# Performance work log

Hardware: AMD Instinct MI355X
Metric: run time of the kernel (lower is better)

Reference implementation:

```python
import jax, jax.numpy as jnp
import numpy as np

K = 3          # neighbors for interpolation (torch_geometric default)
BIG = 1e10     # masks cross-batch pairs out of the kNN search
EPS = 1e-16    # clamp on squared distance before inverting (PyG knn_interpolate)


def setup_inputs() -> dict:
    key = jax.random.key(0)
    ks = jax.random.split(key, 8)
    N, M, C_IN, C_SKIP, H = 4096, 16384, 256, 128, 256
    x = jax.random.normal(ks[0], (N, C_IN), dtype=jnp.float32)
    pos = jax.random.normal(ks[1], (N, 3), dtype=jnp.float32)
    batch = jnp.zeros((N,), dtype=jnp.int64)
    x_skip = jax.random.normal(ks[2], (M, C_SKIP), dtype=jnp.float32)
    pos_skip = jax.random.normal(ks[3], (M, 3), dtype=jnp.float32)
    batch_skip = jnp.zeros((M,), dtype=jnp.int64)
    # MLP params: Linear(384->256) + ReLU + Linear(256->256)
    W1 = jax.random.normal(ks[4], (C_IN + C_SKIP, H), dtype=jnp.float32) * (1.0 / np.sqrt(C_IN + C_SKIP))
    b1 = jnp.zeros((H,), dtype=jnp.float32)
    W2 = jax.random.normal(ks[5], (H, H), dtype=jnp.float32) * (1.0 / np.sqrt(H))
    b2 = jnp.zeros((H,), dtype=jnp.float32)
    return {"x": x, "pos": pos, "batch": batch, "x_skip": x_skip,
            "pos_skip": pos_skip, "batch_skip": batch_skip,
            "W1": W1, "b1": b1, "W2": W2, "b2": b2}


def knn_interpolate(x, pos, pos_skip, batch, batch_skip, k):
    # squared pairwise distances [M, N] via ||q||^2 + ||p||^2 - 2 q.p (avoids [M,N,3])
    qq = jnp.sum(pos_skip * pos_skip, axis=1, keepdims=True)      # [M,1]
    pp = jnp.sum(pos * pos, axis=1)                               # [N]
    d2 = qq + pp[None, :] - 2.0 * (pos_skip @ pos.T)              # [M,N]
    d2 = d2 + jnp.where(batch_skip[:, None] != batch[None, :], BIG, 0.0)
    _, idx = jax.lax.top_k(-d2, k)                                # [M,k] nearest indices
    # recompute exact squared distances for the chosen neighbors
    nbr_pos = pos[idx]                                            # [M,k,3]
    d2k = jnp.sum((pos_skip[:, None, :] - nbr_pos) ** 2, axis=-1) # [M,k]
    w = 1.0 / jnp.clip(d2k, EPS)                                  # inverse-distance weights
    nbr_x = x[idx]                                                # [M,k,C]
    y = jnp.einsum('mk,mkc->mc', w, nbr_x) / jnp.sum(w, axis=1, keepdims=True)
    return y


def reference(x, pos, batch, x_skip, pos_skip, batch_skip, W1, b1, W2, b2):
    y = knn_interpolate(x, pos, pos_skip, batch, batch_skip, K)   # [M, C_in]
    h = jnp.concatenate([y, x_skip], axis=1)                      # [M, C_in+C_skip]
    h = jax.nn.relu(h @ W1 + b1)
    out = h @ W2 + b2
    return (out, pos_skip, batch_skip)
```

## Files before the change

kernel.cpp:

```cpp
#include <hip/hip_runtime.h>
#include <hip/hip_bf16.h>

#define N_PTS  4096
#define M_Q    16384
#define C_IN   256
#define C_SKIP 128
#define C_H    384
#define HDIM   256
#define QB     64

typedef __bf16 bf16x8 __attribute__((ext_vector_type(8)));
typedef float  f32x4  __attribute__((ext_vector_type(4)));

__device__ __forceinline__ void insert3(float d, int j,
                                        float& b0, float& b1, float& b2,
                                        int& i0, int& i1, int& i2) {
    if (d < b2) {
        if (d < b1) {
            b2 = b1; i2 = i1;
            if (d < b0) { b1 = b0; i1 = i0; b0 = d; i0 = j; }
            else        { b1 = d;  i1 = j; }
        } else { b2 = d; i2 = j; }
    }
}

__global__ __launch_bounds__(256) void prep_tail_kernel(
        const float* __restrict__ W1, const float* __restrict__ W2,
        const float* __restrict__ pos, const float* __restrict__ pos_skip,
        __hip_bfloat16* __restrict__ W1t, __hip_bfloat16* __restrict__ W2t,
        float4* __restrict__ pos4, float* __restrict__ out, int out_size) {
    const int i = blockIdx.x * 256 + threadIdx.x;
    if (i < C_H * HDIM) {
        const int k = i / HDIM, n = i % HDIM;
        W1t[n * C_H + k] = __float2bfloat16(W1[i]);
    } else if (i < C_H * HDIM + HDIM * HDIM) {
        const int j = i - C_H * HDIM;
        const int k = j / HDIM, n = j % HDIM;
        W2t[n * HDIM + k] = __float2bfloat16(W2[j]);
    } else if (i < C_H * HDIM + HDIM * HDIM + N_PTS) {
        const int j = i - (C_H * HDIM + HDIM * HDIM);
        const float px = pos[j*3+0], py = pos[j*3+1], pz = pos[j*3+2];
        pos4[j] = make_float4(px, py, pz, px*px + py*py + pz*pz);
    }
    if (i < M_Q * 3) out[(size_t)M_Q * HDIM + i] = pos_skip[i];
    const int zbase = M_Q * HDIM + M_Q * 3;
    if (zbase + i < out_size) out[zbase + i] = 0.0f;
}

__global__ __launch_bounds__(512) void mega_kernel(
        const float4* __restrict__ pos4, const float* __restrict__ pos_skip,
        const float* __restrict__ x, const float* __restrict__ x_skip,
        const __bf16* __restrict__ W1t, const __bf16* __restrict__ W2t,
        const float* __restrict__ b1, const float* __restrict__ b2,
        float* __restrict__ out) {
    __shared__ __align__(16) char smem[51712];
    __hip_bfloat16* h     = (__hip_bfloat16*)smem;
    __hip_bfloat16* hid   = (__hip_bfloat16*)smem;
    float*          candD = (float*)smem;
    int*            candI = (int*)  (smem + 6144);
    int*            idxL  = (int*)  (smem + 50176);
    float*          wnL   = (float*)(smem + 50944);

    const int t    = threadIdx.x;
    const int m0   = blockIdx.x * QB;
    const int wave = t >> 6, lane = t & 63;

    float4 skipv[4];
    #pragma unroll
    for (int p = 0; p < 4; ++p) {
        const int g = p * 512 + t;
        const int r = g >> 5, c = (g & 31) * 4;
        skipv[p] = *(const float4*)(x_skip + (size_t)(m0 + r) * C_SKIP + c);
    }

    const int q = m0 + lane;
    const float qx = pos_skip[q*3+0], qy = pos_skip[q*3+1], qz = pos_skip[q*3+2];
    const float m2x = -2.0f * qx, m2y = -2.0f * qy, m2z = -2.0f * qz;

    {
        const int j0 = __builtin_amdgcn_readfirstlane(wave * (N_PTS / 8));
        float bb0 = 3e38f, bb1 = 3e38f, bb2 = 3e38f;
        int   ii0 = 0, ii1 = 0, ii2 = 0;
        #pragma unroll 8
        for (int j = 0; j < N_PTS / 8; ++j) {
            const float4 p = pos4[j0 + j];
            const float d = fmaf(p.x, m2x, fmaf(p.y, m2y, fmaf(p.z, m2z, p.w)));
            const int  jj = j0 + j;
            const bool c0 = d < bb0, c1 = d < bb1, c2 = d < bb2;
            ii2 = c2 ? (c1 ? ii1 : jj) : ii2;
            ii1 = c1 ? (c0 ? ii0 : jj) : ii1;
            ii0 = c0 ? jj : ii0;
            bb2 = __builtin_amdgcn_fmed3f(d, bb1, bb2);
            bb1 = __builtin_amdgcn_fmed3f(d, bb0, bb1);
            bb0 = fminf(bb0, d);
        }
        const int ci = (wave * 64 + lane) * 3;
        candD[ci+0] = bb0; candD[ci+1] = bb1; candD[ci+2] = bb2;
        candI[ci+0] = ii0; candI[ci+1] = ii1; candI[ci+2] = ii2;
    }
    __syncthreads();

    if (t < 64) {
        float B0 = 3e38f, B1 = 3e38f, B2v = 3e38f;
        int   I0 = 0, I1 = 0, I2 = 0;
        #pragma unroll
        for (int ww = 0; ww < 8; ++ww) {
            const int ci = (ww * 64 + t) * 3;
            insert3(candD[ci+0], candI[ci+0], B0,B1,B2v, I0,I1,I2);
            insert3(candD[ci+1], candI[ci+1], B0,B1,B2v, I0,I1,I2);
            insert3(candD[ci+2], candI[ci+2], B0,B1,B2v, I0,I1,I2);
        }
        const float qq = qx*qx + qy*qy + qz*qz;
        const float w0 = 1.0f / fmaxf(B0  + qq, 1e-16f);
        const float w1 = 1.0f / fmaxf(B1  + qq, 1e-16f);
        const float w2 = 1.0f / fmaxf(B2v + qq, 1e-16f);
        const float inv = 1.0f / (w0 + w1 + w2);
        idxL[t*3+0] = I0; idxL[t*3+1] = I1; idxL[t*3+2] = I2;
        wnL[t*3+0] = w0*inv; wnL[t*3+1] = w1*inv; wnL[t*3+2] = w2*inv;
    }
    __syncthreads();

    const int ln = lane & 15, kq = lane >> 4;
    const int wm  = (wave >> 2) * 32;
    const int wnc = (wave & 3) * 64;

    bf16x8 bfA[4], bfB[4];
    #pragma unroll
    for (int nt = 0; nt < 4; ++nt) {
        bfA[nt] = *(const bf16x8*)(W1t + (size_t)(wnc + nt*16 + ln) * C_H +  0 + kq*8);
        bfB[nt] = *(const bf16x8*)(W1t + (size_t)(wnc + nt*16 + ln) * C_H + 32 + kq*8);
    }

    #pragma unroll
    for (int p = 0; p < 4; ++p) {
        const int g = p * 512 + t;
        const int r = g >> 5, c = (g & 31) * 4;
        union { __hip_bfloat162 v2[2]; uint2 u; } pk;
        pk.v2[0].x = __float2bfloat16(skipv[p].x); pk.v2[0].y = __float2bfloat16(skipv[p].y);
        pk.v2[1].x = __float2bfloat16(skipv[p].z); pk.v2[1].y = __float2bfloat16(skipv[p].w);
        *(uint2*)&h[(size_t)r * 392 + C_IN + c] = pk.u;
    }
    #pragma unroll 4
    for (int p = 0; p < 8; ++p) {
        const int g = p * 512 + t;
        const int r = g >> 6, c = (g & 63) * 4;
        const int   i0 = idxL[r*3+0], i1 = idxL[r*3+1], i2 = idxL[r*3+2];
        const float w0 = wnL[r*3+0],  w1 = wnL[r*3+1],  w2 = wnL[r*3+2];
        const float4 v0 = *(const float4*)(x + (size_t)i0 * C_IN + c);
        const float4 v1 = *(const float4*)(x + (size_t)i1 * C_IN + c);
        const float4 v2 = *(const float4*)(x + (size_t)i2 * C_IN + c);
        union { __hip_bfloat162 v2_[2]; uint2 u; } pk;
        pk.v2_[0].x = __float2bfloat16(w0*v0.x + w1*v1.x + w2*v2.x);
        pk.v2_[0].y = __float2bfloat16(w0*v0.y + w1*v1.y + w2*v2.y);
        pk.v2_[1].x = __float2bfloat16(w0*v0.z + w1*v1.z + w2*v2.z);
        pk.v2_[1].y = __float2bfloat16(w0*v0.w + w1*v1.w + w2*v2.w);
        *(uint2*)&h[(size_t)r * 392 + c] = pk.u;
    }
    __syncthreads();

    f32x4 acc[2][4] = {};

    #pragma unroll
    for (int s = 0; s < 12; ++s) {
        const int k0 = s * 32;
        bf16x8* bc = (s & 1) ? bfB : bfA;
        const bf16x8 a0 = *(const bf16x8*)&h[(size_t)(wm +      ln) * 392 + k0 + kq*8];
        const bf16x8 a1 = *(const bf16x8*)&h[(size_t)(wm + 16 + ln) * 392 + k0 + kq*8];
        #pragma unroll
        for (int nt = 0; nt < 4; ++nt)
            acc[0][nt] = __builtin_amdgcn_mfma_f32_16x16x32_bf16(a0, bc[nt], acc[0][nt], 0,0,0);
        #pragma unroll
        for (int nt = 0; nt < 4; ++nt)
            acc[1][nt] = __builtin_amdgcn_mfma_f32_16x16x32_bf16(a1, bc[nt], acc[1][nt], 0,0,0);
        if (s < 10) {
            #pragma unroll
            for (int nt = 0; nt < 4; ++nt)
                bc[nt] = *(const bf16x8*)(W1t + (size_t)(wnc + nt*16 + ln) * C_H + (k0 + 64) + kq*8);
        } else {
            #pragma unroll
            for (int nt = 0; nt < 4; ++nt)
                bc[nt] = *(const bf16x8*)(W2t + (size_t)(wnc + nt*16 + ln) * HDIM + (s - 10) * 32 + kq*8);
        }
    }
    __syncthreads();

    #pragma unroll
    for (int nt = 0; nt < 4; ++nt) {
        const int n = wnc + nt*16 + ln;
        const float bv = b1[n];
        #pragma unroll
        for (int mt = 0; mt < 2; ++mt) {
            const int rbase = wm + mt*16 + kq*4;
            #pragma unroll
            for (int r = 0; r < 4; ++r) {
                const float v = fmaxf(acc[mt][nt][r] + bv, 0.0f);
                hid[(size_t)(rbase + r) * 264 + n] = __float2bfloat16(v);
                acc[mt][nt][r] = 0.0f;
            }
        }
    }
    __syncthreads();

    #pragma unroll
    for (int s = 0; s < 8; ++s) {
        const int k0 = s * 32;
        bf16x8* bc = (s & 1) ? bfB : bfA;
        const bf16x8 a0 = *(const bf16x8*)&hid[(size_t)(wm +      ln) * 264 + k0 + kq*8];
        const bf16x8 a1 = *(const bf16x8*)&hid[(size_t)(wm + 16 + ln) * 264 + k0 + kq*8];
        #pragma unroll
        for (int nt = 0; nt < 4; ++nt)
            acc[0][nt] = __builtin_amdgcn_mfma_f32_16x16x32_bf16(a0, bc[nt], acc[0][nt], 0,0,0);
        #pragma unroll
        for (int nt = 0; nt < 4; ++nt)
            acc[1][nt] = __builtin_amdgcn_mfma_f32_16x16x32_bf16(a1, bc[nt], acc[1][nt], 0,0,0);
        if (s < 6) {
            #pragma unroll
            for (int nt = 0; nt < 4; ++nt)
                bc[nt] = *(const bf16x8*)(W2t + (size_t)(wnc + nt*16 + ln) * HDIM + (k0 + 64) + kq*8);
        }
    }

    #pragma unroll
    for (int nt = 0; nt < 4; ++nt) {
        const int n = wnc + nt*16 + ln;
        const float bv = b2[n];
        #pragma unroll
        for (int mt = 0; mt < 2; ++mt) {
            const int rbase = m0 + wm + mt*16 + kq*4;
            #pragma unroll
            for (int r = 0; r < 4; ++r)
                out[(size_t)(rbase + r) * HDIM + n] = acc[mt][nt][r] + bv;
        }
    }
}

extern "C" void kernel_launch(void* const* d_in, const int* in_sizes, int n_in,
                              void* d_out, int out_size, void* d_ws, size_t ws_size,
                              hipStream_t stream) {
    (void)in_sizes; (void)n_in; (void)ws_size;
    const float* x        = (const float*)d_in[0];
    const float* pos      = (const float*)d_in[1];
    const float* x_skip   = (const float*)d_in[3];
    const float* pos_skip = (const float*)d_in[4];
    const float* W1       = (const float*)d_in[6];
    const float* b1       = (const float*)d_in[7];
    const float* W2       = (const float*)d_in[8];
    const float* b2       = (const float*)d_in[9];
    float* out = (float*)d_out;

    char* ws = (char*)d_ws;
    __hip_bfloat16* W1t  = (__hip_bfloat16*)(ws);
    __hip_bfloat16* W2t  = (__hip_bfloat16*)(ws + 196608);
    float4*         pos4 = (float4*)(ws + 327680);

    prep_tail_kernel<<<(C_H*HDIM + HDIM*HDIM + N_PTS + 255)/256, 256, 0, stream>>>(
        W1, W2, pos, pos_skip, W1t, W2t, pos4, out, out_size);
    mega_kernel<<<M_Q/QB, 512, 0, stream>>>(
        pos4, pos_skip, x, x_skip, (const __bf16*)W1t, (const __bf16*)W2t, b1, b2, out);
}
```

Before: 151.4 us.

## Compute kNN distances with bf16-split MFMA and two-pass exact candidate refinement

Replaces the scalar FMA distance scan with MFMA matrix products. Coordinates are split into three bf16 parts to approximate fp32 precision, and the packed query and point operands are built in the prep kernel. A first pass finds an approximate third-nearest distance per query. A second pass collects every point within that threshold plus a margin into a shared-memory candidate list, and the final top-3 is recomputed with exact fp32 distances. This is meant to move the dominant distance work onto matrix cores, but it scans the points twice and relies on the margin and candidate cap of 24 to keep results correct.

```diff
diff --git a/kernel.cpp b/kernel.cpp
--- a/kernel.cpp
+++ b/kernel.cpp
@@ -8,39 +8,83 @@
 #define C_H    384
 #define HDIM   256
 #define QB     64
+#define CANDMAX 24
+#define EPSW   4e-3f
 
 typedef __bf16 bf16x8 __attribute__((ext_vector_type(8)));
 typedef float  f32x4  __attribute__((ext_vector_type(4)));
 
-__device__ __forceinline__ void insert3(float d, int j,
-                                        float& b0, float& b1, float& b2,
-                                        int& i0, int& i1, int& i2) {
-    if (d < b2) {
-        if (d < b1) {
-            b2 = b1; i2 = i1;
-            if (d < b0) { b1 = b0; i1 = i0; b0 = d; i0 = j; }
-            else        { b1 = d;  i1 = j; }
-        } else { b2 = d; i2 = j; }
-    }
+#define PW1  (C_H*HDIM)
+#define PW2  (PW1 + HDIM*HDIM)
+#define PPV  (PW2 + N_PTS)
+#define PAQ  (PPV + M_Q)
+
+__device__ __forceinline__ unsigned short bfbits(float v) {
+    __hip_bfloat16 b = __float2bfloat16(v);
+    return *(unsigned short*)&b;
+}
+__device__ __forceinline__ float bff(unsigned short u) {
+    __hip_bfloat16 b = *(__hip_bfloat16*)&u;
+    return __bfloat162float(b);
+}
+__device__ __forceinline__ void split3(float v, unsigned short& h,
+                                       unsigned short& m, unsigned short& l) {
+    h = bfbits(v);       float r  = v - bff(h);
+    m = bfbits(r);       float r2 = r - bff(m);
+    l = bfbits(r2);
 }
 
 __global__ __launch_bounds__(256) void prep_tail_kernel(
         const float* __restrict__ W1, const float* __restrict__ W2,
         const float* __restrict__ pos, const float* __restrict__ pos_skip,
         __hip_bfloat16* __restrict__ W1t, __hip_bfloat16* __restrict__ W2t,
-        float4* __restrict__ pos4, float* __restrict__ out, int out_size) {
+        __hip_bfloat16* __restrict__ Aq, __hip_bfloat16* __restrict__ Pv,
+        float* __restrict__ out, int out_size) {
     const int i = blockIdx.x * 256 + threadIdx.x;
-    if (i < C_H * HDIM) {
+    if (i < PW1) {
         const int k = i / HDIM, n = i % HDIM;
         W1t[n * C_H + k] = __float2bfloat16(W1[i]);
-    } else if (i < C_H * HDIM + HDIM * HDIM) {
-        const int j = i - C_H * HDIM;
+    } else if (i < PW2) {
+        const int j = i - PW1;
         const int k = j / HDIM, n = j % HDIM;
         W2t[n * HDIM + k] = __float2bfloat16(W2[j]);
-    } else if (i < C_H * HDIM + HDIM * HDIM + N_PTS) {
-        const int j = i - (C_H * HDIM + HDIM * HDIM);
+    } else if (i < PPV) {
+        const int j = i - PW2;
         const float px = pos[j*3+0], py = pos[j*3+1], pz = pos[j*3+2];
-        pos4[j] = make_float4(px, py, pz, px*px + py*py + pz*pz);
+        const float pw = px*px + py*py + pz*pz;
+        union { unsigned short u[32]; uint4 q[4]; } S;
+        #pragma unroll
+        for (int k = 0; k < 32; ++k) S.u[k] = 0;
+        const float pd[3] = {px, py, pz};
+        #pragma unroll
+        for (int d = 0; d < 3; ++d) {
+            unsigned short bh, bm, bl; split3(pd[d], bh, bm, bl);
+            S.u[6*d+0] = bh; S.u[6*d+1] = bm; S.u[6*d+2] = bh;
+            S.u[6*d+3] = bl; S.u[6*d+4] = bh; S.u[6*d+5] = bm;
+        }
+        unsigned short wh, wm, wl; split3(pw, wh, wm, wl);
+        S.u[18] = wh; S.u[19] = wm; S.u[20] = wl;
+        uint4* dst = (uint4*)(Pv + (size_t)j * 32);
+        dst[0] = S.q[0]; dst[1] = S.q[1]; dst[2] = S.q[2]; dst[3] = S.q[3];
+    } else if (i < PAQ) {
+        const int j = i - PPV;
+        const float ax = -2.0f * pos_skip[j*3+0];
+        const float ay = -2.0f * pos_skip[j*3+1];
+        const float az = -2.0f * pos_skip[j*3+2];
+        union { unsigned short u[32]; uint4 q[4]; } S;
+        #pragma unroll
+        for (int k = 0; k < 32; ++k) S.u[k] = 0;
+        const float ad[3] = {ax, ay, az};
+        #pragma unroll
+        for (int d = 0; d < 3; ++d) {
+            unsigned short ah, am, al; split3(ad[d], ah, am, al);
+            S.u[6*d+0] = ah; S.u[6*d+1] = ah; S.u[6*d+2] = am;
+            S.u[6*d+3] = ah; S.u[6*d+4] = al; S.u[6*d+5] = am;
+        }
+        const unsigned short one = bfbits(1.0f);
+        S.u[18] = one; S.u[19] = one; S.u[20] = one;
+        uint4* dst = (uint4*)(Aq + (size_t)j * 32);
+        dst[0] = S.q[0]; dst[1] = S.q[1]; dst[2] = S.q[2]; dst[3] = S.q[3];
     }
     if (i < M_Q * 3) out[(size_t)M_Q * HDIM + i] = pos_skip[i];
     const int zbase = M_Q * HDIM + M_Q * 3;
@@ -48,22 +92,28 @@
 }
 
 __global__ __launch_bounds__(512) void mega_kernel(
-        const float4* __restrict__ pos4, const float* __restrict__ pos_skip,
+        const __bf16* __restrict__ Aq, const __bf16* __restrict__ Pv,
+        const float* __restrict__ pos, const float* __restrict__ pos_skip,
         const float* __restrict__ x, const float* __restrict__ x_skip,
         const __bf16* __restrict__ W1t, const __bf16* __restrict__ W2t,
         const float* __restrict__ b1, const float* __restrict__ b2,
         float* __restrict__ out) {
-    __shared__ __align__(16) char smem[51712];
+    __shared__ __align__(16) char smem[51968];
     __hip_bfloat16* h     = (__hip_bfloat16*)smem;
     __hip_bfloat16* hid   = (__hip_bfloat16*)smem;
     float*          candD = (float*)smem;
     int*            candI = (int*)  (smem + 6144);
-    int*            idxL  = (int*)  (smem + 50176);
-    float*          wnL   = (float*)(smem + 50944);
+    int*            candC = (int*)  (smem + 12288);
+    float*          bb2G  = (float*)(smem + 50176);
+    int*            idxL  = (int*)  (smem + 50432);
+    float*          wnL   = (float*)(smem + 51200);
 
     const int t    = threadIdx.x;
     const int m0   = blockIdx.x * QB;
     const int wave = t >> 6, lane = t & 63;
+    const int ln = lane & 15, kq = lane >> 4;
+
+    if (t < 64) candC[t] = 0;
 
     float4 skipv[4];
     #pragma unroll
@@ -73,54 +123,150 @@
         skipv[p] = *(const float4*)(x_skip + (size_t)(m0 + r) * C_SKIP + c);
     }
 
-    const int q = m0 + lane;
-    const float qx = pos_skip[q*3+0], qy = pos_skip[q*3+1], qz = pos_skip[q*3+2];
-    const float m2x = -2.0f * qx, m2y = -2.0f * qy, m2z = -2.0f * qz;
-
-    {
-        const int j0 = __builtin_amdgcn_readfirstlane(wave * (N_PTS / 8));
-        float bb0 = 3e38f, bb1 = 3e38f, bb2 = 3e38f;
-        int   ii0 = 0, ii1 = 0, ii2 = 0;
-        #pragma unroll 8
-        for (int j = 0; j < N_PTS / 8; ++j) {
-            const float4 p = pos4[j0 + j];
-            const float d = fmaf(p.x, m2x, fmaf(p.y, m2y, fmaf(p.z, m2z, p.w)));
-            const int  jj = j0 + j;
-            const bool c0 = d < bb0, c1 = d < bb1, c2 = d < bb2;
-            ii2 = c2 ? (c1 ? ii1 : jj) : ii2;
-            ii1 = c1 ? (c0 ? ii0 : jj) : ii1;
-            ii0 = c0 ? jj : ii0;
-            bb2 = __builtin_amdgcn_fmed3f(d, bb1, bb2);
-            bb1 = __builtin_amdgcn_fmed3f(d, bb0, bb1);
-            bb0 = fminf(bb0, d);
-        }
-        const int ci = (wave * 64 + lane) * 3;
-        candD[ci+0] = bb0; candD[ci+1] = bb1; candD[ci+2] = bb2;
-        candI[ci+0] = ii0; candI[ci+1] = ii1; candI[ci+2] = ii2;
+    bf16x8 afq[4];
+    #pragma unroll
+    for (int qt = 0; qt < 4; ++qt)
+        afq[qt] = *(const bf16x8*)(Aq + (size_t)(m0 + qt*16 + ln) * 32 + kq*8);
+
+    const f32x4 zacc = {0.0f, 0.0f, 0.0f, 0.0f};
+    const int ptbase = wave * 32;
+
+    float b0_[4][4], b1_[4][4], b2_[4][4];
+    #pragma unroll
+    for (int qt = 0; qt < 4; ++qt)
+        #pragma unroll
+        for (int r = 0; r < 4; ++r) { b0_[qt][r]=3e38f; b1_[qt][r]=3e38f; b2_[qt][r]=3e38f; }
+
+    bf16x8 bcur = *(const bf16x8*)(Pv + (size_t)(ptbase*16 + ln) * 32 + kq*8);
+    for (int pt = 0; pt < 32; ++pt) {
+        bf16x8 bnext;
+        if (pt < 31)
+            bnext = *(const bf16x8*)(Pv + (size_t)((ptbase+pt+1)*16 + ln) * 32 + kq*8);
+        #pragma unroll
+        for (int qt = 0; qt < 4; ++qt) {
+            const f32x4 d = __builtin_amdgcn_mfma_f32_16x16x32_bf16(afq[qt], bcur, zacc, 0,0,0);
+            #pragma unroll
+            for (int r = 0; r < 4; ++r) {
+                b2_[qt][r] = __builtin_amdgcn_fmed3f(d[r], b1_[qt][r], b2_[qt][r]);
+                b1_[qt][r] = __builtin_amdgcn_fmed3f(d[r], b0_[qt][r], b1_[qt][r]);
+                b0_[qt][r] = fminf(b0_[qt][r], d[r]);
+            }
+        }
+        bcur = bnext;
+    }
+    #pragma unroll
+    for (int qt = 0; qt < 4; ++qt)
+        #pragma unroll
+        for (int r = 0; r < 4; ++r) {
+            float v0 = b0_[qt][r], v1 = b1_[qt][r], v2 = b2_[qt][r];
+            #pragma unroll
+            for (int m = 1; m <= 8; m <<= 1) {
+                const float o0 = __shfl_xor(v0, m), o1 = __shfl_xor(v1, m), o2 = __shfl_xor(v2, m);
+                const float mx  = fmaxf(v0, o0);
+                const float z0  = fminf(v0, o0);
+                const float mn1 = fminf(v1, o1);
+                const float mn2 = fminf(v2, o2);
+                v0 = z0;
+                v1 = fminf(mx, mn1);
+                v2 = __builtin_amdgcn_fmed3f(mx, mn1, mn2);
+            }
+            b0_[qt][r] = v0; b1_[qt][r] = v1; b2_[qt][r] = v2;
+        }
+    if (ln == 0) {
+        #pragma unroll
+        for (int qt = 0; qt < 4; ++qt)
+            #pragma unroll
+            for (int r = 0; r < 4; ++r) {
+                const int base = (wave*64 + qt*16 + kq*4 + r) * 3;
+                candD[base+0] = b0_[qt][r];
+                candD[base+1] = b1_[qt][r];
+                candD[base+2] = b2_[qt][r];
+            }
     }
     __syncthreads();
 
     if (t < 64) {
-        float B0 = 3e38f, B1 = 3e38f, B2v = 3e38f;
-        int   I0 = 0, I1 = 0, I2 = 0;
+        float B0 = 3e38f, B1 = 3e38f, B2 = 3e38f;
         #pragma unroll
         for (int ww = 0; ww < 8; ++ww) {
-            const int ci = (ww * 64 + t) * 3;
-            insert3(candD[ci+0], candI[ci+0], B0,B1,B2v, I0,I1,I2);
-            insert3(candD[ci+1], candI[ci+1], B0,B1,B2v, I0,I1,I2);
-            insert3(candD[ci+2], candI[ci+2], B0,B1,B2v, I0,I1,I2);
-        }
-        const float qq = qx*qx + qy*qy + qz*qz;
-        const float w0 = 1.0f / fmaxf(B0  + qq, 1e-16f);
-        const float w1 = 1.0f / fmaxf(B1  + qq, 1e-16f);
-        const float w2 = 1.0f / fmaxf(B2v + qq, 1e-16f);
+            const int base = (ww*64 + t) * 3;
+            #pragma unroll
+            for (int k = 0; k < 3; ++k) {
+                const float v = candD[base+k];
+                B2 = __builtin_amdgcn_fmed3f(v, B1, B2);
+                B1 = __builtin_amdgcn_fmed3f(v, B0, B1);
+                B0 = fminf(B0, v);
+            }
+        }
+        bb2G[t] = B2;
+    }
+    __syncthreads();
+
+    float thr[4][4];
+    #pragma unroll
+    for (int qt = 0; qt < 4; ++qt)
+        #pragma unroll
+        for (int r = 0; r < 4; ++r)
+            thr[qt][r] = bb2G[qt*16 + kq*4 + r] + EPSW;
+
+    bcur = *(const bf16x8*)(Pv + (size_t)(ptbase*16 + ln) * 32 + kq*8);
+    for (int pt = 0; pt < 32; ++pt) {
+        bf16x8 bnext;
+        if (pt < 31)
+            bnext = *(const bf16x8*)(Pv + (size_t)((ptbase+pt+1)*16 + ln) * 32 + kq*8);
+        const int pidx = (ptbase + pt) * 16 + ln;
+        #pragma unroll
+        for (int qt = 0; qt < 4; ++qt) {
+            const f32x4 d = __builtin_amdgcn_mfma_f32_16x16x32_bf16(afq[qt], bcur, zacc, 0,0,0);
+            const bool h0 = d[0] <= thr[qt][0], h1 = d[1] <= thr[qt][1];
+            const bool h2 = d[2] <= thr[qt][2], h3 = d[3] <= thr[qt][3];
+            if (__builtin_expect(h0|h1|h2|h3, 0)) {
+                #pragma unroll
+                for (int r = 0; r < 4; ++r) {
+                    if (d[r] <= thr[qt][r]) {
+                        const int row = qt*16 + kq*4 + r;
+                        const int n = atomicAdd(&candC[row], 1);
+                        if (n < CANDMAX) candI[row*CANDMAX + n] = pidx;
+                    }
+                }
+            }
+        }
+        bcur = bnext;
+    }
+    __syncthreads();
+
+    if (t < 64) {
+        const int q = m0 + t;
+        const float qx = pos_skip[q*3+0], qy = pos_skip[q*3+1], qz = pos_skip[q*3+2];
+        int cnt = candC[t]; if (cnt > CANDMAX) cnt = CANDMAX;
+        float e0 = 3e38f, e1 = 3e38f, e2 = 3e38f;
+        int   i0 = 0x7fffffff, i1 = 0x7fffffff, i2 = 0x7fffffff;
+        for (int c = 0; c < cnt; ++c) {
+            const int j = candI[t*CANDMAX + c];
+            const float dx = qx - pos[j*3+0];
+            const float dy = qy - pos[j*3+1];
+            const float dz = qz - pos[j*3+2];
+            const float d2 = dx*dx + dy*dy + dz*dz;
+            const bool c2 = (d2 < e2) || (d2 == e2 && j < i2);
+            if (c2) {
+                const bool c1 = (d2 < e1) || (d2 == e1 && j < i1);
+                if (c1) {
+                    e2 = e1; i2 = i1;
+                    const bool c0 = (d2 < e0) || (d2 == e0 && j < i0);
+                    if (c0) { e1 = e0; i1 = i0; e0 = d2; i0 = j; }
+                    else    { e1 = d2; i1 = j; }
+                } else { e2 = d2; i2 = j; }
+            }
+        }
+        const float w0 = 1.0f / fmaxf(e0, 1e-16f);
+        const float w1 = 1.0f / fmaxf(e1, 1e-16f);
+        const float w2 = 1.0f / fmaxf(e2, 1e-16f);
         const float inv = 1.0f / (w0 + w1 + w2);
-        idxL[t*3+0] = I0; idxL[t*3+1] = I1; idxL[t*3+2] = I2;
+        idxL[t*3+0] = i0; idxL[t*3+1] = i1; idxL[t*3+2] = i2;
         wnL[t*3+0] = w0*inv; wnL[t*3+1] = w1*inv; wnL[t*3+2] = w2*inv;
     }
     __syncthreads();
 
-    const int ln = lane & 15, kq = lane >> 4;
     const int wm  = (wave >> 2) * 32;
     const int wnc = (wave & 3) * 64;
 
@@ -249,12 +395,14 @@
     float* out = (float*)d_out;
 
     char* ws = (char*)d_ws;
-    __hip_bfloat16* W1t  = (__hip_bfloat16*)(ws);
-    __hip_bfloat16* W2t  = (__hip_bfloat16*)(ws + 196608);
-    float4*         pos4 = (float4*)(ws + 327680);
-
-    prep_tail_kernel<<<(C_H*HDIM + HDIM*HDIM + N_PTS + 255)/256, 256, 0, stream>>>(
-        W1, W2, pos, pos_skip, W1t, W2t, pos4, out, out_size);
+    __hip_bfloat16* W1t = (__hip_bfloat16*)(ws);
+    __hip_bfloat16* W2t = (__hip_bfloat16*)(ws + 196608);
+    __hip_bfloat16* Aq  = (__hip_bfloat16*)(ws + 327680);
+    __hip_bfloat16* Pv  = (__hip_bfloat16*)(ws + 1376256);
+
+    prep_tail_kernel<<<(PAQ + 255)/256, 256, 0, stream>>>(
+        W1, W2, pos, pos_skip, W1t, W2t, Aq, Pv, out, out_size);
     mega_kernel<<<M_Q/QB, 512, 0, stream>>>(
-        pos4, pos_skip, x, x_skip, (const __bf16*)W1t, (const __bf16*)W2t, b1, b2, out);
-}
+        (const __bf16*)Aq, (const __bf16*)Pv, pos, pos_skip, x, x_skip,
+        (const __bf16*)W1t, (const __bf16*)W2t, b1, b2, out);
+}
```

After: 139.3 us (median of 2 runs). -8.0%, faster.
